# Kernel tuning notes

Measured on AMD Instinct MI355X. Metric: run time of the kernel, lower is better.

The kernel has to match this reference:

```python
import jax, jax.numpy as jnp
import numpy as np

B = 131072
H = 192          # hidden_dim
NH = 4           # attention heads
HD = H // NH     # head dim = 48
MEM = 16         # resonance memory slots
GRID = 64        # 8x8 SOFM grid
DIMS = (("vib", 64), ("aco", 256), ("tmp", 128))


def setup_inputs() -> dict:
    key = jax.random.key(0)
    ks = iter(jax.random.split(key, 64))

    def nrm(shape, scale=0.02):
        return jax.random.normal(next(ks), shape, dtype=jnp.float32) * scale

    inp = {}
    inp["x_vib"] = jax.random.normal(next(ks), (B, 64), dtype=jnp.float32)
    inp["x_aco"] = jax.random.normal(next(ks), (B, 256), dtype=jnp.float32)
    inp["x_tmp"] = jax.random.normal(next(ks), (B, 128), dtype=jnp.float32)
    for m, d in DIMS:
        inp[f"enc_w_{m}"] = nrm((d, H))
        inp[f"enc_b_{m}"] = jnp.zeros((H,), jnp.float32)
        inp[f"enc_g_{m}"] = jnp.ones((H,), jnp.float32)
        inp[f"enc_bb_{m}"] = jnp.zeros((H,), jnp.float32)
    inp["fus_w"] = nrm((3 * H, H))
    inp["fus_b"] = jnp.zeros((H,), jnp.float32)
    inp["fus_g"] = jnp.ones((H,), jnp.float32)
    inp["fus_bb"] = jnp.zeros((H,), jnp.float32)
    inp["res_wq"] = nrm((3, H, H))
    inp["res_wk"] = nrm((3, H, H))
    inp["res_wv"] = nrm((3, H, H))
    inp["res_wo"] = nrm((3, H, H))
    inp["res_bq"] = jnp.zeros((3, H), jnp.float32)
    inp["res_bk"] = jnp.zeros((3, H), jnp.float32)
    inp["res_bv"] = jnp.zeros((3, H), jnp.float32)
    inp["res_bo"] = jnp.zeros((3, H), jnp.float32)
    inp["res_mem"] = nrm((3, MEM, H), 1.0)
    inp["grid"] = nrm((GRID, H), 1.0)
    inp["out_w"] = nrm((H, 6))
    inp["out_b"] = jnp.zeros((6,), jnp.float32)
    return inp


def _ln(x, g, b):
    m = x.mean(-1, keepdims=True)
    v = ((x - m) ** 2).mean(-1, keepdims=True)
    return (x - m) / jnp.sqrt(v + 1e-5) * g + b


def reference(x_vib, x_aco, x_tmp,
              enc_w_vib, enc_b_vib, enc_g_vib, enc_bb_vib,
              enc_w_aco, enc_b_aco, enc_g_aco, enc_bb_aco,
              enc_w_tmp, enc_b_tmp, enc_g_tmp, enc_bb_tmp,
              fus_w, fus_b, fus_g, fus_bb,
              res_wq, res_wk, res_wv, res_wo,
              res_bq, res_bk, res_bv, res_bo, res_mem,
              grid, out_w, out_b):
    # per-modality Linear + LayerNorm + GELU encoders
    feats = []
    for x, w, b, g, bb in ((x_vib, enc_w_vib, enc_b_vib, enc_g_vib, enc_bb_vib),
                           (x_aco, enc_w_aco, enc_b_aco, enc_g_aco, enc_bb_aco),
                           (x_tmp, enc_w_tmp, enc_b_tmp, enc_g_tmp, enc_bb_tmp)):
        feats.append(jax.nn.gelu(_ln(x @ w + b, g, bb), approximate=False))
    fused = jnp.concatenate(feats, axis=-1)                         # [B, 3H]
    fused = jax.nn.gelu(_ln(fused @ fus_w + fus_b, fus_g, fus_bb), approximate=False)

    # 3 adaptive resonance layers: cross-attention over a 16-slot memory bank
    scale = 1.0 / jnp.sqrt(jnp.float32(HD))
    for i in range(3):
        q = (fused @ res_wq[i] + res_bq[i]).reshape(-1, NH, HD)     # [B, h, d]
        k = (res_mem[i] @ res_wk[i] + res_bk[i]).reshape(MEM, NH, HD)
        v = (res_mem[i] @ res_wv[i] + res_bv[i]).reshape(MEM, NH, HD)
        scores = jnp.einsum("bhd,mhd->bhm", q, k) * scale           # [B, h, 16]
        attn = jax.nn.softmax(scores, axis=-1)
        o = jnp.einsum("bhm,mhd->bhd", attn, v).reshape(-1, H)
        fused = o @ res_wo[i] + res_bo[i]

    # SOFM: nearest-grid-vector lookup (squared dist has same argmin as cdist)
    d2 = (fused ** 2).sum(-1, keepdims=True) - 2.0 * (fused @ grid.T) + (grid ** 2).sum(-1)
    winners = jnp.argmin(d2, axis=1)                                # [B]
    fused = grid[winners]                                           # [B, H]

    pooled = fused.mean(axis=0)                                     # [H]
    out = pooled @ out_w + out_b                                    # [6]
    sig = jax.nn.sigmoid(out)
    # wear, remaining_life(relu), failure_prob, quality, confidence, anomaly
    return jnp.stack([sig[0], jax.nn.relu(out[1]), sig[2], sig[3], sig[4], sig[5]])
```

## Files before the change

### kernel.cpp

```cpp
#include <hip/hip_runtime.h>
#include <hip/hip_bf16.h>
#include <math.h>

typedef unsigned short ushort_t;
typedef __attribute__((ext_vector_type(8))) short short8;
typedef __attribute__((ext_vector_type(4))) float f32x4;

#define B_TOTAL 131072

#define OFF_VIB 0
#define OFF_ACO 12288
#define OFF_TMP 61440
#define OFF_FUS 86016
#define OFF_WK 196608
#define OFF_M 208896
#define F32_BYTE_OFF 442368
#define F_KV 0
#define F_VV 9216
#define F_VPP 18432
#define F_WKF 55296
#define F_BSF 92160
#define F_BATTN 92352
#define F_BG 92544
#define F_CNT 92608

__device__ __forceinline__ ushort_t f2bu_prep(float f) {
  union { float f; unsigned u; } c; c.f = f;
  unsigned u = c.u;
  unsigned r = (u + 0x7fffu + ((u >> 16) & 1u)) >> 16;
  return (ushort_t)r;
}
__device__ __forceinline__ ushort_t f2bu(float f) {
  __hip_bfloat16 h = __float2bfloat16(f);
  return *(ushort_t*)&h;
}
__device__ __forceinline__ float fastrcp(float x) { return __builtin_amdgcn_rcpf(x); }
__device__ __forceinline__ float gelu_fast(float x) {
  float u = 0.7978845608f * x * (1.0f + 0.044715f * x * x);
  float E = exp2f(2.88539008f * u);
  float t = 1.0f - 2.0f * fastrcp(E + 1.0f);
  return 0.5f * x * (1.0f + t);
}
#define MFMA16(a, b, c) __builtin_amdgcn_mfma_f32_16x16x32_bf16(a, b, c, 0, 0, 0)

__device__ __forceinline__ void gload16(const void* g, void* l) {
  __builtin_amdgcn_global_load_lds((const __attribute__((address_space(1))) void*)g,
                                   (__attribute__((address_space(3))) void*)l, 16, 0, 0);
}

__global__ void prep_weights(const float* __restrict__ ev, const float* __restrict__ ea,
                             const float* __restrict__ et, const float* __restrict__ fw,
                             ushort_t* __restrict__ ws) {
  int tid = blockIdx.x * blockDim.x + threadIdx.x;
  int nth = gridDim.x * blockDim.x;
  for (int i = tid; i < 12288; i += nth) {
    int n = i >> 6, kin = i & 63;
    int k = 8 * ((kin >> 3) ^ (n & 7)) + (kin & 7);
    ws[OFF_VIB + i] = f2bu_prep(ev[k * 192 + n]);
  }
  for (int i = tid; i < 49152; i += nth) {
    int ck = i / 12288, rem = i % 12288, n = rem >> 6, kin = rem & 63;
    int k = ck * 64 + 8 * ((kin >> 3) ^ (n & 7)) + (kin & 7);
    ws[OFF_ACO + i] = f2bu_prep(ea[k * 192 + n]);
  }
  for (int i = tid; i < 24576; i += nth) {
    int ck = i / 12288, rem = i % 12288, n = rem >> 6, kin = rem & 63;
    int k = ck * 64 + 8 * ((kin >> 3) ^ (n & 7)) + (kin & 7);
    ws[OFF_TMP + i] = f2bu_prep(et[k * 192 + n]);
  }
  for (int i = tid; i < 110592; i += nth) {
    int ck = i / 12288, rem = i % 12288, n = rem >> 6, kin = rem & 63;
    int k = ck * 64 + 8 * ((kin >> 3) ^ (n & 7)) + (kin & 7);
    ws[OFF_FUS + i] = f2bu_prep(fw[k * 192 + n]);
  }
}

__global__ void prep_kv1(const float* __restrict__ rwk, const float* __restrict__ rwv,
                         const float* __restrict__ rbk, const float* __restrict__ rbv,
                         const float* __restrict__ rmem, float* __restrict__ wsf,
                         unsigned* __restrict__ cnt) {
  int tid = blockIdx.x * blockDim.x + threadIdx.x;
  int nth = gridDim.x * blockDim.x;
  for (int idx = tid; idx < 18432; idx += nth) {
    int bank = idx / 9216, r = idx % 9216;
    int i = r / 3072, q = r % 3072, s = q / 192, d = q % 192;
    const float* w  = (bank ? rwv : rwk) + i * 36864;
    const float* bs = (bank ? rbv : rbk) + i * 192;
    const float* mm = rmem + i * 3072 + s * 192;
    float acc = bs[d];
    for (int kk = 0; kk < 192; ++kk) acc += mm[kk] * w[kk * 192 + d];
    wsf[bank * 9216 + (i * 16 + s) * 192 + d] = acc;
  }
  for (int g = tid; g < 64; g += nth) cnt[g] = 0u;
}

__global__ void prep_kv2(const float* __restrict__ rwq, const float* __restrict__ rbq,
                         const float* __restrict__ rwo, float* __restrict__ wsf,
                         ushort_t* __restrict__ ws) {
  int tid = blockIdx.x * blockDim.x + threadIdx.x;
  int nth = gridDim.x * blockDim.x;
  const float scale = 0.144337567297406441f;
  const float* Kv = wsf + F_KV;
  const float* Vv = wsf + F_VV;
  float* WKf = wsf + F_WKF;
  float* Vpp = wsf + F_VPP;
  float* bSf = wsf + F_BSF;
  for (int idx = tid; idx < 36864; idx += nth) {
    int i = idx / 12288, rem = idx % 12288, n = rem / 192, k = rem % 192;
    int h = n >> 4, s = n & 15;
    const float* kvp = Kv + (i * 16 + s) * 192 + h * 48;
    const float* wqp = rwq + i * 36864 + k * 192 + h * 48;
    float acc = 0.f;
    for (int d = 0; d < 48; ++d) acc += wqp[d] * kvp[d];
    WKf[idx] = scale * acc;
  }
  for (int idx = tid; idx < 12288; idx += nth) {
    int ck = idx >> 12, r2 = idx & 4095, n = r2 >> 6, kin = r2 & 63;
    int k = ck * 64 + 8 * ((kin >> 3) ^ (n & 7)) + (kin & 7);
    int h = n >> 4, s = n & 15;
    const float* kvp = Kv + s * 192 + h * 48;
    const float* wqp = rwq + k * 192 + h * 48;
    float acc = 0.f;
    for (int d = 0; d < 48; ++d) acc += wqp[d] * kvp[d];
    ws[OFF_WK + idx] = f2bu_prep(scale * acc);
  }
  for (int idx = tid; idx < 36864; idx += nth) {
    int i = idx / 12288, rem = idx % 12288, n = rem / 192, dcol = rem % 192;
    int h = n >> 4, s = n & 15;
    const float* vvp = Vv + (i * 16 + s) * 192 + h * 48;
    const float* wop = rwo + i * 36864 + (h * 48) * 192 + dcol;
    float acc = 0.f;
    for (int d = 0; d < 48; ++d) acc += vvp[d] * wop[d * 192];
    Vpp[idx] = acc;
  }
  for (int idx = tid; idx < 192; idx += nth) {
    int i = idx >> 6, n = idx & 63, h = n >> 4, s = n & 15;
    const float* kvp = Kv + (i * 16 + s) * 192 + h * 48;
    const float* bqp = rbq + i * 192 + h * 48;
    float acc = 0.f;
    for (int d = 0; d < 48; ++d) acc += bqp[d] * kvp[d];
    bSf[idx] = scale * acc;
  }
}

__global__ void prep_kv3(const float* __restrict__ rbo, const float* __restrict__ gr,
                         float* __restrict__ wsf, ushort_t* __restrict__ ws) {
  int tid = blockIdx.x * blockDim.x + threadIdx.x;
  int nth = gridDim.x * blockDim.x;
  const float* Vpp = wsf + F_VPP;
  const float* WKf = wsf + F_WKF;
  const float* bSf = wsf + F_BSF;
  for (int idx = tid; idx < 8192; idx += nth) {
    int l = idx >> 12, rem = idx & 4095, n = rem >> 6, kin = rem & 63;
    int k = 8 * ((kin >> 3) ^ (n & 7)) + (kin & 7);
    const float* vp = Vpp + l * 12288 + k * 192;
    const float* wp = WKf + (l + 1) * 12288 + n * 192;
    float acc = 0.f;
    for (int t = 0; t < 192; ++t) acc += vp[t] * wp[t];
    ws[OFF_M + l * 4096 + n * 64 + kin] = f2bu_prep(acc);
  }
  for (int idx = tid; idx < 4096; idx += nth) {
    int n = idx >> 6, kin = idx & 63;
    int k = 8 * ((kin >> 3) ^ (n & 7)) + (kin & 7);
    const float* vp = Vpp + 2 * 12288 + k * 192;
    const float* gp = gr + n * 192;
    float acc = 0.f;
    for (int t = 0; t < 192; ++t) acc += vp[t] * gp[t];
    ws[OFF_M + 8192 + n * 64 + kin] = f2bu_prep(acc);
  }
  for (int idx = tid; idx < 192; idx += nth) {
    int l = idx >> 6, n = idx & 63;
    float acc = bSf[l * 64 + n];
    if (l > 0) {
      const float* wp = WKf + l * 12288 + n * 192;
      const float* bo = rbo + (l - 1) * 192;
      for (int t = 0; t < 192; ++t) acc += bo[t] * wp[t];
    }
    wsf[F_BATTN + idx] = acc;
  }
  for (int g = tid; g < 64; g += nth) {
    const float* gp = gr + g * 192;
    const float* bo = rbo + 2 * 192;
    float a = 0.f, s = 0.f;
    for (int t = 0; t < 192; ++t) { a += bo[t] * gp[t]; s += gp[t] * gp[t]; }
    wsf[F_BG + g] = a - 0.5f * s;
  }
}

__device__ __forceinline__ void stage_to(ushort_t* dst, const ushort_t* src, int nseg,
                                         int wave, int lane) {
  for (int s = wave; s < nseg; s += 4)
    gload16(src + (s << 9) + lane * 8, dst + (s << 9));
}

__device__ __forceinline__ const ushort_t* chunk_ptr(const ushort_t* wsu, int g, int* nseg) {
  *nseg = 24;
  if (g < 1)            return wsu + OFF_VIB;
  g -= 1;  if (g < 3)   return wsu + OFF_FUS + g * 12288;
  g -= 3;  if (g < 4)   return wsu + OFF_ACO + g * 12288;
  g -= 4;  if (g < 3)   return wsu + OFF_FUS + 36864 + g * 12288;
  g -= 3;  if (g < 2)   return wsu + OFF_TMP + g * 12288;
  g -= 2;  if (g < 3)   return wsu + OFF_FUS + 73728 + g * 12288;
  g -= 3;  if (g < 3)   { *nseg = 8; return wsu + OFF_WK + g * 4096; }
  g -= 3;  if (g < 3)   { *nseg = 8; return wsu + OFF_M + g * 4096; }
  *nseg = 0; return wsu;
}

__device__ __forceinline__ void phase_begin(const ushort_t* wsu, ushort_t (*Wb)[12288],
                                            int gph, int wave, int lane) {
  __syncthreads();
  int nseg; const ushort_t* ns = chunk_ptr(wsu, gph + 1, &nseg);
  if (nseg) stage_to(&Wb[(gph + 1) & 1][0], ns, nseg, wave, lane);
}

__device__ __forceinline__ short8 cvt8(float4 a, float4 b) {
  short8 v;
  v[0] = (short)f2bu(a.x); v[1] = (short)f2bu(a.y); v[2] = (short)f2bu(a.z); v[3] = (short)f2bu(a.w);
  v[4] = (short)f2bu(b.x); v[5] = (short)f2bu(b.y); v[6] = (short)f2bu(b.z); v[7] = (short)f2bu(b.w);
  return v;
}

template<int NPH>
__device__ __forceinline__ void enc_gemm(const float* __restrict__ x, int row0,
    const ushort_t* wsu, ushort_t (*Wb)[12288], int* gph, f32x4* accE,
    int m, int gq, int wave, int lane) {
  const int KF = NPH * 64;
  const float* p0 = x + (size_t)row0 * KF + gq * 8;
  float4 ca0 = *(const float4*)(p0);
  float4 ca1 = *(const float4*)(p0 + 4);
#pragma unroll
  for (int ph = 0; ph < NPH; ++ph) {
    phase_begin(wsu, Wb, *gph, wave, lane);
    const ushort_t* Wc = &Wb[*gph & 1][0];
#pragma unroll
    for (int ks = 0; ks < 2; ++ks) {
      int sl = ks * 4 + gq;
      short8 a = cvt8(ca0, ca1);
      int nk = ph * 64 + ks * 32 + 32;
      if (nk < KF) {
        ca0 = *(const float4*)(p0 + nk);
        ca1 = *(const float4*)(p0 + nk + 4);
      }
#pragma unroll
      for (int t = 0; t < 12; ++t) {
        int n = t * 16 + m;
        short8 b = *(const short8*)(Wc + n * 64 + ((sl ^ (n & 7)) << 3));
        accE[t] = MFMA16(b, a, accE[t]);
      }
    }
    ++*gph;
  }
}

__device__ __forceinline__ void lds_gemm(const ushort_t* Ab, const ushort_t* wsu,
    ushort_t (*Wb)[12288], int* gph, f32x4* acc, int wc0, int m, int gq,
    int wave, int lane) {
#pragma unroll
  for (int ph = 0; ph < 3; ++ph) {
    phase_begin(wsu, Wb, *gph, wave, lane);
    const ushort_t* Wc = &Wb[*gph & 1][0];
#pragma unroll
    for (int ks = 0; ks < 2; ++ks) {
      int sl = ks * 4 + gq;
      short8 b0, b1, b2;
      {
        int n0 = wc0 + m, n1 = wc0 + 16 + m, n2 = wc0 + 32 + m;
        b0 = *(const short8*)(Wc + n0 * 64 + ((sl ^ (n0 & 7)) << 3));
        b1 = *(const short8*)(Wc + n1 * 64 + ((sl ^ (n1 & 7)) << 3));
        b2 = *(const short8*)(Wc + n2 * 64 + ((sl ^ (n2 & 7)) << 3));
      }
#pragma unroll
      for (int mt = 0; mt < 4; ++mt) {
        int r = mt * 16 + m;
        short8 a = *(const short8*)(Ab + r * 192 + ((ph * 8 + (sl ^ (r & 7))) << 3));
        acc[mt * 3 + 0] = MFMA16(b0, a, acc[mt * 3 + 0]);
        acc[mt * 3 + 1] = MFMA16(b1, a, acc[mt * 3 + 1]);
        acc[mt * 3 + 2] = MFMA16(b2, a, acc[mt * 3 + 2]);
      }
    }
    ++*gph;
  }
}

__device__ __forceinline__ void ln_gelu_enc(f32x4* acc, const float* __restrict__ bias,
    const float* __restrict__ gam, const float* __restrict__ bet,
    ushort_t* __restrict__ Ab, int rloc, int gq) {
  float s = 0.f, q = 0.f;
#pragma unroll
  for (int t = 0; t < 12; ++t) {
    float4 bv = *(const float4*)(bias + t * 16 + gq * 4);
#pragma unroll
    for (int j = 0; j < 4; ++j) {
      float v = acc[t][j] + ((const float*)&bv)[j];
      acc[t][j] = v; s += v; q += v * v;
    }
  }
  s += __shfl_xor(s, 16, 64); q += __shfl_xor(q, 16, 64);
  s += __shfl_xor(s, 32, 64); q += __shfl_xor(q, 32, 64);
  float mean = s * (1.0f / 192.0f);
  float var = q * (1.0f / 192.0f) - mean * mean;
  float rstd = rsqrtf(var + 1e-5f);
#pragma unroll
  for (int t = 0; t < 12; ++t) {
    int colb = t * 16 + gq * 4;
    float4 ga = *(const float4*)(gam + colb);
    float4 be = *(const float4*)(bet + colb);
    ushort_t o[4];
#pragma unroll
    for (int j = 0; j < 4; ++j) {
      float y = (acc[t][j] - mean) * rstd * ((const float*)&ga)[j] + ((const float*)&be)[j];
      o[j] = f2bu(gelu_fast(y));
    }
    int off = rloc * 192 + (((colb >> 3) ^ (rloc & 7)) << 3) + (colb & 7);
    *(uint2*)(Ab + off) = *(uint2*)o;
  }
}

__device__ __forceinline__ void ln_gelu_fus(f32x4* acc, const float* __restrict__ bias,
    const float* __restrict__ gam, const float* __restrict__ bet,
    ushort_t* __restrict__ Ab, float2 (*scr)[4], int wave, int wc0, int m, int gq) {
  float4 bv[3];
#pragma unroll
  for (int t = 0; t < 3; ++t) bv[t] = *(const float4*)(bias + wc0 + t * 16 + gq * 4);
#pragma unroll
  for (int mt = 0; mt < 4; ++mt) {
    float s = 0.f, q = 0.f;
#pragma unroll
    for (int t = 0; t < 3; ++t)
#pragma unroll
      for (int j = 0; j < 4; ++j) {
        float v = acc[mt * 3 + t][j] + ((const float*)&bv[t])[j];
        acc[mt * 3 + t][j] = v; s += v; q += v * v;
      }
    s += __shfl_xor(s, 16, 64); q += __shfl_xor(q, 16, 64);
    s += __shfl_xor(s, 32, 64); q += __shfl_xor(q, 32, 64);
    if (gq == 0) scr[mt * 16 + m][wave] = (float2){s, q};
  }
  __syncthreads();
#pragma unroll
  for (int mt = 0; mt < 4; ++mt) {
    int row = mt * 16 + m;
    float s = 0.f, q = 0.f;
#pragma unroll
    for (int w = 0; w < 4; ++w) { float2 p = scr[row][w]; s += p.x; q += p.y; }
    float mean = s * (1.0f / 192.0f);
    float var = q * (1.0f / 192.0f) - mean * mean;
    float rstd = rsqrtf(var + 1e-5f);
#pragma unroll
    for (int t = 0; t < 3; ++t) {
      int colb = wc0 + t * 16 + gq * 4;
      float4 ga = *(const float4*)(gam + colb);
      float4 be = *(const float4*)(bet + colb);
      ushort_t o[4];
#pragma unroll
      for (int j = 0; j < 4; ++j) {
        float y = (acc[mt * 3 + t][j] - mean) * rstd * ((const float*)&ga)[j] + ((const float*)&be)[j];
        o[j] = f2bu(gelu_fast(y));
      }
      int off = row * 192 + (((colb >> 3) ^ (row & 7)) << 3) + (colb & 7);
      *(uint2*)(Ab + off) = *(uint2*)o;
    }
  }
}

__device__ __forceinline__ void softmax_to_P(f32x4* accS, const float* __restrict__ bptr,
    ushort_t* __restrict__ Pb, int w16, int m, int gq) {
  float4 b4 = *(const float4*)(bptr + w16 + gq * 4);
  const int gnum = (w16 + gq * 4) >> 3;
#pragma unroll
  for (int mt = 0; mt < 4; ++mt) {
    float e[4]; float mx = -3.0e38f;
#pragma unroll
    for (int j = 0; j < 4; ++j) { e[j] = accS[mt][j] + ((const float*)&b4)[j]; mx = fmaxf(mx, e[j]); }
    mx = fmaxf(mx, __shfl_xor(mx, 16, 64));
    mx = fmaxf(mx, __shfl_xor(mx, 32, 64));
    float sm = 0.f;
#pragma unroll
    for (int j = 0; j < 4; ++j) { e[j] = exp2f((e[j] - mx) * 1.44269504f); sm += e[j]; }
    sm += __shfl_xor(sm, 16, 64);
    sm += __shfl_xor(sm, 32, 64);
    float inv = fastrcp(sm);
    ushort_t p4[4];
#pragma unroll
    for (int j = 0; j < 4; ++j) p4[j] = f2bu(e[j] * inv);
    int r = mt * 16 + m;
    *(uint2*)(Pb + r * 64 + ((gnum ^ (r & 7)) << 3) + (gq & 1) * 4) = *(uint2*)p4;
  }
}

__global__ __launch_bounds__(256) __attribute__((amdgpu_waves_per_eu(2))) void arn_main(
    const float* __restrict__ xv, const float* __restrict__ xa, const float* __restrict__ xt,
    const ushort_t* __restrict__ wsu, const float* __restrict__ battn,
    const float* __restrict__ bG, unsigned* __restrict__ counts,
    const float* __restrict__ ebv, const float* __restrict__ egv, const float* __restrict__ ebbv,
    const float* __restrict__ eba, const float* __restrict__ ega, const float* __restrict__ ebba,
    const float* __restrict__ ebt, const float* __restrict__ egt, const float* __restrict__ ebbt,
    const float* __restrict__ fb, const float* __restrict__ fg, const float* __restrict__ fbb) {
  __shared__ __align__(16) ushort_t Abuf[64 * 192 + 64];
  __shared__ __align__(16) ushort_t Wbuf[2][12288];
  __shared__ float2 lnscr[64][4];
  __shared__ unsigned hist[64];

  const int tid = threadIdx.x, lane = tid & 63, wave = tid >> 6;
  const int m = lane & 15, gq = lane >> 4;
  const int wc0 = wave * 48;
  const int w16 = wave * 16;
  const int growbase = blockIdx.x * 64;

  if (tid < 64) { hist[tid] = 0u; Abuf[12288 + tid] = 0; }

  int gph = 0;
  { int nseg; const ushort_t* s0 = chunk_ptr(wsu, 0, &nseg); stage_to(&Wbuf[0][0], s0, nseg, wave, lane); }

  const int row0 = growbase + w16 + m;
  const int rloc = w16 + m;
  f32x4 accF[12];
#pragma unroll
  for (int t = 0; t < 12; ++t) accF[t] = (f32x4){0.f, 0.f, 0.f, 0.f};

  {
    f32x4 accE[12];
#pragma unroll
    for (int t = 0; t < 12; ++t) accE[t] = (f32x4){0.f, 0.f, 0.f, 0.f};
    enc_gemm<1>(xv, row0, wsu, Wbuf, &gph, accE, m, gq, wave, lane);
    ln_gelu_enc(accE, ebv, egv, ebbv, Abuf, rloc, gq);
  }
  lds_gemm(Abuf, wsu, Wbuf, &gph, accF, wc0, m, gq, wave, lane);

  {
    f32x4 accE[12];
#pragma unroll
    for (int t = 0; t < 12; ++t) accE[t] = (f32x4){0.f, 0.f, 0.f, 0.f};
    enc_gemm<4>(xa, row0, wsu, Wbuf, &gph, accE, m, gq, wave, lane);
    ln_gelu_enc(accE, eba, ega, ebba, Abuf, rloc, gq);
  }
  lds_gemm(Abuf, wsu, Wbuf, &gph, accF, wc0, m, gq, wave, lane);

  {
    f32x4 accE[12];
#pragma unroll
    for (int t = 0; t < 12; ++t) accE[t] = (f32x4){0.f, 0.f, 0.f, 0.f};
    enc_gemm<2>(xt, row0, wsu, Wbuf, &gph, accE, m, gq, wave, lane);
    ln_gelu_enc(accE, ebt, egt, ebbt, Abuf, rloc, gq);
  }
  lds_gemm(Abuf, wsu, Wbuf, &gph, accF, wc0, m, gq, wave, lane);
  ln_gelu_fus(accF, fb, fg, fbb, Abuf, lnscr, wave, wc0, m, gq);

  {
    f32x4 accS[4];
#pragma unroll
    for (int t = 0; t < 4; ++t) accS[t] = (f32x4){0.f, 0.f, 0.f, 0.f};
#pragma unroll
    for (int ph = 0; ph < 3; ++ph) {
      phase_begin(wsu, Wbuf, gph, wave, lane);
      const ushort_t* Wc = &Wbuf[gph & 1][0];
      int n = w16 + m;
#pragma unroll
      for (int ks = 0; ks < 2; ++ks) {
        int sl = ks * 4 + gq;
        short8 b = *(const short8*)(Wc + n * 64 + ((sl ^ (n & 7)) << 3));
#pragma unroll
        for (int mt = 0; mt < 4; ++mt) {
          int r = mt * 16 + m;
          short8 a = *(const short8*)(Abuf + r * 192 + ((ph * 8 + (sl ^ (r & 7))) << 3));
          accS[mt] = MFMA16(b, a, accS[mt]);
        }
      }
      ++gph;
    }
    softmax_to_P(accS, battn, &Wbuf[(gph - 1) & 1][8192], w16, m, gq);

#pragma unroll
    for (int l = 1; l <= 2; ++l) {
      const ushort_t* Pprev = &Wbuf[(gph & 1) ^ 1][8192];
#pragma unroll
      for (int t = 0; t < 4; ++t) accS[t] = (f32x4){0.f, 0.f, 0.f, 0.f};
      phase_begin(wsu, Wbuf, gph, wave, lane);
      const ushort_t* Wc = &Wbuf[gph & 1][0];
      int n = w16 + m;
#pragma unroll
      for (int ks = 0; ks < 2; ++ks) {
        int sl = ks * 4 + gq;
        short8 b = *(const short8*)(Wc + n * 64 + ((sl ^ (n & 7)) << 3));
#pragma unroll
        for (int mt = 0; mt < 4; ++mt) {
          int r = mt * 16 + m;
          short8 a = *(const short8*)(Pprev + r * 64 + ((sl ^ (r & 7)) << 3));
          accS[mt] = MFMA16(b, a, accS[mt]);
        }
      }
      ++gph;
      softmax_to_P(accS, battn + l * 64, &Wbuf[(gph - 1) & 1][8192], w16, m, gq);
    }

    {
      const ushort_t* P3 = &Wbuf[(gph & 1) ^ 1][8192];
      f32x4 accG[4];
#pragma unroll
      for (int t = 0; t < 4; ++t) accG[t] = (f32x4){0.f, 0.f, 0.f, 0.f};
      phase_begin(wsu, Wbuf, gph, wave, lane);
      const ushort_t* Wc = &Wbuf[gph & 1][0];
      int r = w16 + m;
#pragma unroll
      for (int ks = 0; ks < 2; ++ks) {
        int sl = ks * 4 + gq;
        short8 a = *(const short8*)(P3 + r * 64 + ((sl ^ (r & 7)) << 3));
#pragma unroll
        for (int nt = 0; nt < 4; ++nt) {
          int n = nt * 16 + m;
          short8 b = *(const short8*)(Wc + n * 64 + ((sl ^ (n & 7)) << 3));
          accG[nt] = MFMA16(b, a, accG[nt]);
        }
      }
      ++gph;
      float bv = -3.0e38f; int bi = 64;
#pragma unroll
      for (int nt = 0; nt < 4; ++nt) {
        int gb = nt * 16 + gq * 4;
        float4 g4 = *(const float4*)(bG + gb);
#pragma unroll
        for (int j = 0; j < 4; ++j) {
          float v = accG[nt][j] + ((const float*)&g4)[j];
          int g = gb + j;
          bool take = (v > bv);
          bv = take ? v : bv; bi = take ? g : bi;
        }
      }
#pragma unroll
      for (int off = 16; off < 64; off <<= 1) {
        float ov = __shfl_xor(bv, off, 64);
        int oi = __shfl_xor(bi, off, 64);
        bool take = (ov > bv) || (ov == bv && oi < bi);
        bv = take ? ov : bv; bi = take ? oi : bi;
      }
      if (gq == 0) atomicAdd(&hist[bi], 1u);
    }
  }
  __syncthreads();
  if (tid < 64 && hist[tid]) atomicAdd(&counts[tid], hist[tid]);
}

__global__ void arn_finish(const unsigned* __restrict__ counts, const float* __restrict__ gr,
                           const float* __restrict__ ow, const float* __restrict__ ob,
                           float* __restrict__ out) {
  __shared__ float pooled[192];
  __shared__ float cf[64];
  int t = threadIdx.x;
  if (t < 64) cf[t] = (float)counts[t];
  __syncthreads();
  float s = 0.f;
  for (int g = 0; g < 64; ++g) s += cf[g] * gr[g * 192 + t];
  pooled[t] = s * (1.0f / (float)B_TOTAL);
  __syncthreads();
  if (t < 6) {
    float o = ob[t];
    for (int j = 0; j < 192; ++j) o += pooled[j] * ow[j * 6 + t];
    out[t] = (t == 1) ? fmaxf(o, 0.f) : 1.f / (1.f + expf(-o));
  }
}

extern "C" void kernel_launch(void* const* d_in, const int* in_sizes, int n_in,
                              void* d_out, int out_size, void* d_ws, size_t ws_size,
                              hipStream_t stream) {
  (void)in_sizes; (void)n_in; (void)out_size; (void)ws_size;
  const float* xv   = (const float*)d_in[0];
  const float* xa   = (const float*)d_in[1];
  const float* xt   = (const float*)d_in[2];
  const float* ewv  = (const float*)d_in[3];
  const float* ebv  = (const float*)d_in[4];
  const float* egv  = (const float*)d_in[5];
  const float* ebbv = (const float*)d_in[6];
  const float* ewa  = (const float*)d_in[7];
  const float* eba  = (const float*)d_in[8];
  const float* ega  = (const float*)d_in[9];
  const float* ebba = (const float*)d_in[10];
  const float* ewt  = (const float*)d_in[11];
  const float* ebt  = (const float*)d_in[12];
  const float* egt  = (const float*)d_in[13];
  const float* ebbt = (const float*)d_in[14];
  const float* fw   = (const float*)d_in[15];
  const float* fb   = (const float*)d_in[16];
  const float* fg   = (const float*)d_in[17];
  const float* fbb  = (const float*)d_in[18];
  const float* rwq  = (const float*)d_in[19];
  const float* rwk  = (const float*)d_in[20];
  const float* rwv  = (const float*)d_in[21];
  const float* rwo  = (const float*)d_in[22];
  const float* rbq  = (const float*)d_in[23];
  const float* rbk  = (const float*)d_in[24];
  const float* rbv  = (const float*)d_in[25];
  const float* rbo  = (const float*)d_in[26];
  const float* rmem = (const float*)d_in[27];
  const float* grid = (const float*)d_in[28];
  const float* ow   = (const float*)d_in[29];
  const float* ob   = (const float*)d_in[30];

  ushort_t* wsu = (ushort_t*)d_ws;
  float* wsf = (float*)((char*)d_ws + F32_BYTE_OFF);
  float* battn = wsf + F_BATTN;
  float* bG    = wsf + F_BG;
  unsigned* cnt = (unsigned*)(wsf + F_CNT);

  prep_weights<<<dim3(256), dim3(256), 0, stream>>>(ewv, ewa, ewt, fw, wsu);
  prep_kv1<<<dim3(80), dim3(256), 0, stream>>>(rwk, rwv, rbk, rbv, rmem, wsf, cnt);
  prep_kv2<<<dim3(120), dim3(256), 0, stream>>>(rwq, rbq, rwo, wsf, wsu);
  prep_kv3<<<dim3(64), dim3(256), 0, stream>>>(rbo, grid, wsf, wsu);
  arn_main<<<dim3(2048), dim3(256), 0, stream>>>(xv, xa, xt, wsu, battn, bG, cnt,
      ebv, egv, ebbv, eba, ega, ebba, ebt, egt, ebbt, fb, fg, fbb);
  arn_finish<<<dim3(1), dim3(192), 0, stream>>>(cnt, grid, ow, ob, (float*)d_out);
}
```

Measured before the change: 218.8 us.

## Merge attention weight chunks into single stages and use sigmoid GELU approximation

Repacks the first-layer score weights into one 192-wide chunk and stages the three memory matrices together, so the resonance stage needs two weight staging phases instead of seven, with fewer barriers. The softmax P buffers and memory weights now sit in fixed slices of the double buffer. The tanh GELU is replaced by the cheaper x*sigmoid(1.702x) form, which saves instructions but changes the numerics slightly. stage_to is unrolled to a fixed six segments per wave.

```diff
diff --git a/kernel.cpp b/kernel.cpp
--- a/kernel.cpp
+++ b/kernel.cpp
@@ -36,10 +36,7 @@
 }
 __device__ __forceinline__ float fastrcp(float x) { return __builtin_amdgcn_rcpf(x); }
 __device__ __forceinline__ float gelu_fast(float x) {
-  float u = 0.7978845608f * x * (1.0f + 0.044715f * x * x);
-  float E = exp2f(2.88539008f * u);
-  float t = 1.0f - 2.0f * fastrcp(E + 1.0f);
-  return 0.5f * x * (1.0f + t);
+  return x * fastrcp(1.0f + exp2f(-2.45546465f * x));
 }
 #define MFMA16(a, b, c) __builtin_amdgcn_mfma_f32_16x16x32_bf16(a, b, c, 0, 0, 0)
 
@@ -115,8 +112,8 @@
     WKf[idx] = scale * acc;
   }
   for (int idx = tid; idx < 12288; idx += nth) {
-    int ck = idx >> 12, r2 = idx & 4095, n = r2 >> 6, kin = r2 & 63;
-    int k = ck * 64 + 8 * ((kin >> 3) ^ (n & 7)) + (kin & 7);
+    int n = idx / 192, rem = idx % 192, kb = rem >> 6, kin = rem & 63;
+    int k = kb * 64 + 8 * ((kin >> 3) ^ (n & 7)) + (kin & 7);
     int h = n >> 4, s = n & 15;
     const float* kvp = Kv + s * 192 + h * 48;
     const float* wqp = rwq + k * 192 + h * 48;
@@ -187,10 +184,12 @@
   }
 }
 
-__device__ __forceinline__ void stage_to(ushort_t* dst, const ushort_t* src, int nseg,
-                                         int wave, int lane) {
-  for (int s = wave; s < nseg; s += 4)
+__device__ __forceinline__ void stage_to(ushort_t* dst, const ushort_t* src, int wave, int lane) {
+#pragma unroll
+  for (int j = 0; j < 6; ++j) {
+    int s = wave + j * 4;
     gload16(src + (s << 9) + lane * 8, dst + (s << 9));
+  }
 }
 
 __device__ __forceinline__ const ushort_t* chunk_ptr(const ushort_t* wsu, int g, int* nseg) {
@@ -201,8 +200,8 @@
   g -= 4;  if (g < 3)   return wsu + OFF_FUS + 36864 + g * 12288;
   g -= 3;  if (g < 2)   return wsu + OFF_TMP + g * 12288;
   g -= 2;  if (g < 3)   return wsu + OFF_FUS + 73728 + g * 12288;
-  g -= 3;  if (g < 3)   { *nseg = 8; return wsu + OFF_WK + g * 4096; }
-  g -= 3;  if (g < 3)   { *nseg = 8; return wsu + OFF_M + g * 4096; }
+  g -= 3;  if (g < 1)   return wsu + OFF_WK;
+  g -= 1;  if (g < 1)   return wsu + OFF_M;
   *nseg = 0; return wsu;
 }
 
@@ -210,7 +209,7 @@
                                             int gph, int wave, int lane) {
   __syncthreads();
   int nseg; const ushort_t* ns = chunk_ptr(wsu, gph + 1, &nseg);
-  if (nseg) stage_to(&Wb[(gph + 1) & 1][0], ns, nseg, wave, lane);
+  if (nseg) stage_to(&Wb[(gph + 1) & 1][0], ns, wave, lane);
 }
 
 __device__ __forceinline__ short8 cvt8(float4 a, float4 b) {
@@ -410,7 +409,7 @@
   if (tid < 64) { hist[tid] = 0u; Abuf[12288 + tid] = 0; }
 
   int gph = 0;
-  { int nseg; const ushort_t* s0 = chunk_ptr(wsu, 0, &nseg); stage_to(&Wbuf[0][0], s0, nseg, wave, lane); }
+  { int nseg; const ushort_t* s0 = chunk_ptr(wsu, 0, &nseg); stage_to(&Wbuf[0][0], s0, wave, lane); }
 
   const int row0 = growbase + w16 + m;
   const int rloc = w16 + m;
@@ -450,56 +449,55 @@
     f32x4 accS[4];
 #pragma unroll
     for (int t = 0; t < 4; ++t) accS[t] = (f32x4){0.f, 0.f, 0.f, 0.f};
-#pragma unroll
-    for (int ph = 0; ph < 3; ++ph) {
-      phase_begin(wsu, Wbuf, gph, wave, lane);
-      const ushort_t* Wc = &Wbuf[gph & 1][0];
+    phase_begin(wsu, Wbuf, gph, wave, lane);
+    {
+      const ushort_t* Wc = &Wbuf[0][0];
+      int n = w16 + m;
+#pragma unroll
+      for (int ks = 0; ks < 6; ++ks) {
+        int kb = ks >> 1, sl = (ks & 1) * 4 + gq;
+        short8 b = *(const short8*)(Wc + n * 192 + ((kb * 8 + (sl ^ (n & 7))) << 3));
+#pragma unroll
+        for (int mt = 0; mt < 4; ++mt) {
+          int r = mt * 16 + m;
+          short8 a = *(const short8*)(Abuf + r * 192 + ((kb * 8 + (sl ^ (r & 7))) << 3));
+          accS[mt] = MFMA16(b, a, accS[mt]);
+        }
+      }
+      ++gph;
+    }
+    __syncthreads();
+    softmax_to_P(accS, battn, &Wbuf[0][0], w16, m, gq);
+    __syncthreads();
+
+#pragma unroll
+    for (int l = 1; l <= 2; ++l) {
+      const ushort_t* Mc = &Wbuf[1][(l - 1) * 4096];
+      const ushort_t* Pp = &Wbuf[0][(l - 1) * 4096];
+#pragma unroll
+      for (int t = 0; t < 4; ++t) accS[t] = (f32x4){0.f, 0.f, 0.f, 0.f};
       int n = w16 + m;
 #pragma unroll
       for (int ks = 0; ks < 2; ++ks) {
         int sl = ks * 4 + gq;
-        short8 b = *(const short8*)(Wc + n * 64 + ((sl ^ (n & 7)) << 3));
+        short8 b = *(const short8*)(Mc + n * 64 + ((sl ^ (n & 7)) << 3));
 #pragma unroll
         for (int mt = 0; mt < 4; ++mt) {
           int r = mt * 16 + m;
-          short8 a = *(const short8*)(Abuf + r * 192 + ((ph * 8 + (sl ^ (r & 7))) << 3));
+          short8 a = *(const short8*)(Pp + r * 64 + ((sl ^ (r & 7)) << 3));
           accS[mt] = MFMA16(b, a, accS[mt]);
         }
       }
-      ++gph;
-    }
-    softmax_to_P(accS, battn, &Wbuf[(gph - 1) & 1][8192], w16, m, gq);
-
-#pragma unroll
-    for (int l = 1; l <= 2; ++l) {
-      const ushort_t* Pprev = &Wbuf[(gph & 1) ^ 1][8192];
-#pragma unroll
-      for (int t = 0; t < 4; ++t) accS[t] = (f32x4){0.f, 0.f, 0.f, 0.f};
-      phase_begin(wsu, Wbuf, gph, wave, lane);
-      const ushort_t* Wc = &Wbuf[gph & 1][0];
-      int n = w16 + m;
-#pragma unroll
-      for (int ks = 0; ks < 2; ++ks) {
-        int sl = ks * 4 + gq;
-        short8 b = *(const short8*)(Wc + n * 64 + ((sl ^ (n & 7)) << 3));
-#pragma unroll
-        for (int mt = 0; mt < 4; ++mt) {
-          int r = mt * 16 + m;
-          short8 a = *(const short8*)(Pprev + r * 64 + ((sl ^ (r & 7)) << 3));
-          accS[mt] = MFMA16(b, a, accS[mt]);
-        }
-      }
-      ++gph;
-      softmax_to_P(accS, battn + l * 64, &Wbuf[(gph - 1) & 1][8192], w16, m, gq);
+      softmax_to_P(accS, battn + l * 64, &Wbuf[0][l * 4096], w16, m, gq);
+      __syncthreads();
     }
 
     {
-      const ushort_t* P3 = &Wbuf[(gph & 1) ^ 1][8192];
+      const ushort_t* Mc = &Wbuf[1][8192];
+      const ushort_t* P3 = &Wbuf[0][8192];
       f32x4 accG[4];
 #pragma unroll
       for (int t = 0; t < 4; ++t) accG[t] = (f32x4){0.f, 0.f, 0.f, 0.f};
-      phase_begin(wsu, Wbuf, gph, wave, lane);
-      const ushort_t* Wc = &Wbuf[gph & 1][0];
       int r = w16 + m;
 #pragma unroll
       for (int ks = 0; ks < 2; ++ks) {
@@ -508,11 +506,10 @@
 #pragma unroll
         for (int nt = 0; nt < 4; ++nt) {
           int n = nt * 16 + m;
-          short8 b = *(const short8*)(Wc + n * 64 + ((sl ^ (n & 7)) << 3));
+          short8 b = *(const short8*)(Mc + n * 64 + ((sl ^ (n & 7)) << 3));
           accG[nt] = MFMA16(b, a, accG[nt]);
         }
       }
-      ++gph;
       float bv = -3.0e38f; int bi = 64;
 #pragma unroll
       for (int nt = 0; nt < 4; ++nt) {
```

Measured after the change: 204.7 us. 6.4% less time.
